# Kernel optimization log

Hardware: AMD Instinct MI355X
Metric: run time of the kernel (lower is better)

The kernel has to match this reference:

```python
import jax, jax.numpy as jnp
import numpy as np

NS = 6   # stuff classes
NT = 4   # thing classes
B, N, H, W, ROI = 2, 32, 768, 768, 28
C = NS + NT
NEG = -100.0


def setup_inputs():
    key = jax.random.key(0)
    k1, k2, k3, k4, k5, k6, k7 = jax.random.split(key, 7)
    sem_logits = jax.random.normal(k1, (B, C, H, W), dtype=jnp.float32)
    roi_msk_logits = jax.random.normal(k2, (B, N, NT, ROI, ROI), dtype=jnp.float32)
    y0 = jax.random.uniform(k3, (B, N), minval=0.0, maxval=H - 240.0)
    x0 = jax.random.uniform(k4, (B, N), minval=0.0, maxval=W - 240.0)
    hb = jax.random.uniform(k5, (B, N), minval=40.0, maxval=200.0)
    wb = jax.random.uniform(k6, (B, N), minval=40.0, maxval=200.0)
    bbx = jnp.stack([y0, x0, y0 + hb, x0 + wb], axis=-1).astype(jnp.float32)
    cls = jax.random.randint(k7, (B, N), 0, NT, dtype=jnp.int32)
    return {"sem_logits": sem_logits, "roi_msk_logits": roi_msk_logits, "bbx": bbx, "cls": cls}


def _fuse_logits(sem_logits, roi_msk_logits, bbx, cls):
    """Float part of Pofusion_ONNX.forward -> po_logits [B, NS+N, H, W]."""
    Bb, Cc, Hh, Ww = sem_logits.shape
    Nn = bbx.shape[1]
    R = roi_msk_logits.shape[-1]
    yy = jnp.arange(Hh)
    xx = jnp.arange(Ww)
    # per-box mask logits of its predicted class: [B,N,R,R]
    msk = jnp.take_along_axis(roi_msk_logits, cls[:, :, None, None, None], axis=2)[:, :, 0]
    stuff = sem_logits[:, :NS]  # [B,NS,H,W]
    y0 = jnp.floor(bbx[..., 0]).astype(jnp.int32)
    x0 = jnp.floor(bbx[..., 1]).astype(jnp.int32)
    y1 = jnp.floor(bbx[..., 2]).astype(jnp.int32)
    x1 = jnp.floor(bbx[..., 3]).astype(jnp.int32)
    # ---- po_process_semantic_logits: instance canvas (uses round()+1 on max corner) ----
    y1r = (jnp.round(bbx[..., 2]) + 1.0).astype(jnp.int32)
    x1r = (jnp.round(bbx[..., 3]) + 1.0).astype(jnp.int32)
    in_y_s = (yy[None, None, :] >= y0[..., None]) & (yy[None, None, :] < y1r[..., None])  # [B,N,H]
    in_x_s = (xx[None, None, :] >= x0[..., None]) & (xx[None, None, :] < x1r[..., None])  # [B,N,W]
    thing_logit = jnp.take_along_axis(sem_logits, (cls + NS)[:, :, None, None], axis=1)   # [B,N,H,W]
    inst = jnp.where(in_y_s[:, :, :, None] & in_x_s[:, :, None, :], thing_logit, NEG)
    # ---- po_process_mask_logits: bilinear resize (align_corners=False) + paste ----
    h = jnp.maximum(y1 - y0 + 1, 1).astype(jnp.float32)
    w = jnp.maximum(x1 - x0 + 1, 1).astype(jnp.float32)
    ys = jnp.maximum(y0, 0); ye = jnp.minimum(y1 + 1, Hh)
    xs = jnp.maximum(x0, 0); xe = jnp.minimum(x1 + 1, Ww)
    in_y_m = (yy[None, None, :] >= ys[..., None]) & (yy[None, None, :] < ye[..., None])
    in_x_m = (xx[None, None, :] >= xs[..., None]) & (xx[None, None, :] < xe[..., None])
    # source coords, PyTorch half-pixel convention with lower clamp at 0
    sy = (yy[None, None, :].astype(jnp.float32) - y0[..., None] + 0.5) * (R / h[..., None]) - 0.5
    sx = (xx[None, None, :].astype(jnp.float32) - x0[..., None] + 0.5) * (R / w[..., None]) - 0.5
    sy = jnp.clip(sy, 0.0, R - 1.0)
    sx = jnp.clip(sx, 0.0, R - 1.0)
    iy0 = jnp.floor(sy).astype(jnp.int32); iy1 = jnp.minimum(iy0 + 1, R - 1); wy = sy - iy0
    ix0 = jnp.floor(sx).astype(jnp.int32); ix1 = jnp.minimum(ix0 + 1, R - 1); wx = sx - ix0
    # separable bilinear: rows first (cheap [B,N,H,R] intermediate), then columns
    m0 = jnp.take_along_axis(msk, iy0[:, :, :, None], axis=2)
    m1 = jnp.take_along_axis(msk, iy1[:, :, :, None], axis=2)
    m_y = m0 * (1.0 - wy[..., None]) + m1 * wy[..., None]          # [B,N,H,R]
    c0 = jnp.take_along_axis(m_y, ix0[:, :, None, :], axis=3)
    c1 = jnp.take_along_axis(m_y, ix1[:, :, None, :], axis=3)
    resized = c0 * (1.0 - wx[:, :, None, :]) + c1 * wx[:, :, None, :]  # [B,N,H,W]
    mask_canvas = jnp.where(in_y_m[:, :, :, None] & in_x_m[:, :, None, :], resized, NEG)
    combined = (jax.nn.sigmoid(inst) + jax.nn.sigmoid(mask_canvas)) * (inst + mask_canvas)
    return jnp.concatenate([stuff, combined], axis=1)  # [B, NS+N, H, W]


def _post(po_logits, sem_logits, cls):
    """po_assign_class_label + po_generate_seamless_output (min_stuff_area=0)."""
    b3 = jnp.arange(B)[:, None, None]
    b2 = jnp.arange(B)[:, None]
    po_pred = jnp.argmax(po_logits, axis=1)   # argmax(softmax) == argmax(logits)
    sem_pred = jnp.argmax(sem_logits, axis=1)
    thing = po_pred >= NS
    k = jnp.clip(po_pred - NS, 0, N - 1)      # instance (box) id per pixel
    # per-instance histogram of sem_pred over its region (regions are disjoint)
    hist = jnp.zeros((B, N, C), jnp.int32).at[b3, k, sem_pred].add(thing.astype(jnp.int32))
    total = hist.sum(-1)
    present = total > 0
    sem_max = jnp.argmax(hist, axis=-1).astype(jnp.int32)  # first max == torch unique order
    max_cnt = hist.max(-1)
    tmp = cls + NS
    br1 = sem_max == tmp
    br2 = (~br1) & (2 * max_cnt >= total) & (sem_max < NS) & present  # max/total >= 0.5
    sem_label = jnp.where(br2, sem_max, tmp)
    kept = present & ~br2
    idx = jnp.cumsum(present.astype(jnp.int32), axis=1) - 1  # rank among present ids
    inst_label = jnp.where(kept, idx, -1)
    po_sem = jnp.where(thing, sem_label[b3, k], po_pred.astype(jnp.int32))
    po_inst = jnp.where(thing, inst_label[b3, k], -1)
    # ---- seamless output ----
    sp = jnp.zeros((B, NS), jnp.int32).at[b3, jnp.clip(po_sem, 0, NS - 1)].add((po_sem < NS).astype(jnp.int32))
    stuff_present = sp > 0
    stuff_rank = jnp.cumsum(stuff_present.astype(jnp.int32), axis=1) - 1
    n_stuff = stuff_present.sum(1).astype(jnp.int32)  # [B]
    v = jnp.where(kept, idx, N)
    present_v = (jnp.zeros((B, N + 1), jnp.int32).at[b2, v].add(1) > 0)[:, :N]
    rank_v = jnp.cumsum(present_v.astype(jnp.int32), axis=1) - 1
    seam_inst = 1 + n_stuff[:, None, None] + rank_v[b3, jnp.clip(po_inst, 0, N - 1)]
    seam_stuff = stuff_rank[b3, jnp.clip(po_sem, 0, NS - 1)] + 1
    seam = jnp.where(po_inst >= 0, seam_inst, jnp.where(po_sem < NS, seam_stuff, 0))
    po_pred_seamless = seam.reshape(B * H, W).astype(jnp.int32)  # torch cat over batch
    # padded class list [255, sorted stuff classes..., kept instance classes...]
    L = 1 + NS + N
    po_cls = jnp.full((B, L + 1), -1, jnp.int32).at[:, 0].set(255)
    stuff_pos = jnp.where(stuff_present, 1 + stuff_rank, L)  # L = dump slot
    po_cls = po_cls.at[b2, stuff_pos].set(jnp.broadcast_to(jnp.arange(NS, dtype=jnp.int32), (B, NS)))
    rank_k = jnp.cumsum(kept.astype(jnp.int32), axis=1) - 1
    inst_pos = jnp.where(kept, 1 + n_stuff[:, None] + rank_k, L)
    po_cls = po_cls.at[b2, inst_pos].set(tmp)
    po_cls = po_cls[:, :L]
    valid_len = (1 + n_stuff + kept.sum(1)).astype(jnp.int32)
    po_iscrowd = jnp.where(jnp.arange(L)[None, :] < valid_len[:, None], 0, -1).astype(jnp.int32)
    return po_pred_seamless, po_cls, po_iscrowd, valid_len


def reference(sem_logits, roi_msk_logits, bbx, cls):
    po_logits = _fuse_logits(sem_logits, roi_msk_logits, bbx, cls)
    return _post(po_logits, sem_logits, cls)
```

## Files before the change

kernel.cpp:

```cpp
#include <hip/hip_runtime.h>
#include <math.h>

#define NSs 6
#define NTs 4
#define Bb  2
#define Nn  32
#define Hh  768
#define Ww  768
#define Rr  28
#define Cch 10
#define NCH 38
#define HW  (Hh*Ww)
#define NEGD (-100.0)
#define NEGF (-100.0f)
#define NKEY (Nn*Cch + NSs)

struct InstP {
  int y0, x0, y1r, x1r;
  int ys, ye, xs, xe;
  float sc_y, sc_x;
  int tc;
  int mskoff;
};

__device__ __forceinline__ double sigd(double x) { return 1.0 / (1.0 + exp(-x)); }
__device__ __forceinline__ float  sigf(float x)  { return __fdividef(1.0f, 1.0f + __expf(-x)); }

__device__ __forceinline__ int fuse_px(
    int y, int x, const float (&ch)[Cch], unsigned rel,
    const InstP* __restrict__ spar, const float* __restrict__ roi,
    double EPS, int* smp_out)
{
  int smp = 0; float smv = ch[0];
#pragma unroll
  for (int c = 1; c < Cch; c++) if (ch[c] > smv) { smv = ch[c]; smp = c; }
  *smp_out = smp;

  double m = (double)ch[0]; int pidx = 0;
#pragma unroll
  for (int c = 1; c < NSs; c++) { double v = (double)ch[c]; if (v > m) { m = v; pidx = c; } }

  int next_ch = NSs;
  while (rel) {
    int n = __ffs(rel) - 1; rel &= rel - 1;
    int chn_ = NSs + n;
    if (chn_ > next_ch && EPS > m) { m = EPS; pidx = next_ch; }
    next_ch = chn_ + 1;
    const InstP p = spar[n];
    bool in_i = (y >= p.y0) && (y < p.y1r) && (x >= p.x0) && (x < p.x1r);
    bool in_m = (y >= p.ys) && (y < p.ye)  && (x >= p.xs) && (x < p.xe);
    bool in_any = in_i || in_m;
    if (__any(in_any)) {
      if (in_any) {
        int tcl = p.tc;
        float tl = (tcl == 6) ? ch[6] : (tcl == 7) ? ch[7] : (tcl == 8) ? ch[8] : ch[9];
        double iv = in_i ? (double)tl : NEGD;
        double mv = NEGD;
        if (in_m) {
          double syv = ((double)(y - p.y0) + 0.5) * (double)p.sc_y - 0.5;
          double sxv = ((double)(x - p.x0) + 0.5) * (double)p.sc_x - 0.5;
          syv = fmin(fmax(syv, 0.0), 27.0);
          sxv = fmin(fmax(sxv, 0.0), 27.0);
          int iy0 = (int)syv, ix0 = (int)sxv;
          int iy1 = min(iy0 + 1, 27), ix1 = min(ix0 + 1, 27);
          double wy = syv - (double)iy0, wx = sxv - (double)ix0;
          const float* mp = roi + p.mskoff;
          double m00 = (double)mp[iy0*Rr + ix0];
          double m01 = (double)mp[iy0*Rr + ix1];
          double m10 = (double)mp[iy1*Rr + ix0];
          double m11 = (double)mp[iy1*Rr + ix1];
          double c0 = m00*(1.0 - wy) + m10*wy;
          double c1 = m01*(1.0 - wy) + m11*wy;
          mv = c0*(1.0 - wx) + c1*wx;
        }
        double s2 = iv + mv;
        if (fmax(2.0*s2, 0.0) > m) {
          double val = (sigd(iv) + sigd(mv)) * s2;
          if (val > m) { m = val; pidx = chn_; }
        }
      } else {
        if (EPS > m) { m = EPS; pidx = chn_; }
      }
    } else {
      if (EPS > m) { m = EPS; pidx = chn_; }
    }
  }
  if (next_ch < NCH && EPS > m) { m = EPS; pidx = next_ch; }
  return pidx;
}

#define TOL_E 5e-4f
#define TOL_A 1e-3f
#define TOL_P 2e-3f

__device__ __forceinline__ int fuse_px_f32(
    int y, int x, const float (&ch)[Cch], unsigned rel,
    const InstP* __restrict__ spar, const float* __restrict__ roi,
    float EPSf, bool* certain)
{
  float m1 = ch[0]; int pidx = 0; bool wapprox = false;
  float m2x = -1e30f, m2a = -1e30f;

#define UPD_EXACT(v_, idx_) do { float _v = (v_); \
    if (_v > m1) { if (wapprox) m2a = fmaxf(m2a, m1); else m2x = fmaxf(m2x, m1); \
                   m1 = _v; pidx = (idx_); wapprox = false; } \
    else m2x = fmaxf(m2x, _v); } while (0)
#define UPD_APPROX(v_, idx_) do { float _v = (v_); \
    if (_v > m1) { if (wapprox) m2a = fmaxf(m2a, m1); else m2x = fmaxf(m2x, m1); \
                   m1 = _v; pidx = (idx_); wapprox = true; } \
    else m2a = fmaxf(m2a, _v); } while (0)

#pragma unroll
  for (int c = 1; c < NSs; c++) UPD_EXACT(ch[c], c);

  int next_ch = NSs;
  while (rel) {
    int n = __ffs(rel) - 1; rel &= rel - 1;
    int chn_ = NSs + n;
    if (chn_ > next_ch) UPD_EXACT(EPSf, next_ch);
    next_ch = chn_ + 1;
    const InstP p = spar[n];
    bool in_i = (y >= p.y0) && (y < p.y1r) && (x >= p.x0) && (x < p.x1r);
    bool in_m = (y >= p.ys) && (y < p.ye)  && (x >= p.xs) && (x < p.xe);
    bool in_any = in_i || in_m;
    if (__any(in_any)) {
      if (in_any) {
        int tcl = p.tc;
        float tl = (tcl == 6) ? ch[6] : (tcl == 7) ? ch[7] : (tcl == 8) ? ch[8] : ch[9];
        float iv = in_i ? tl : NEGF;
        float mv = NEGF;
        if (in_m) {
          float syv = ((float)(y - p.y0) + 0.5f) * p.sc_y - 0.5f;
          float sxv = ((float)(x - p.x0) + 0.5f) * p.sc_x - 0.5f;
          syv = fminf(fmaxf(syv, 0.0f), 27.0f);
          sxv = fminf(fmaxf(sxv, 0.0f), 27.0f);
          int iy0 = (int)syv, ix0 = (int)sxv;
          int iy1 = min(iy0 + 1, 27), ix1 = min(ix0 + 1, 27);
          float wy = syv - (float)iy0, wx = sxv - (float)ix0;
          const float* mp = roi + p.mskoff;
          float m00 = mp[iy0*Rr + ix0];
          float m01 = mp[iy0*Rr + ix1];
          float m10 = mp[iy1*Rr + ix0];
          float m11 = mp[iy1*Rr + ix1];
          float c0 = m00*(1.0f - wy) + m10*wy;
          float c1 = m01*(1.0f - wy) + m11*wy;
          mv = c0*(1.0f - wx) + c1*wx;
        }
        float s2 = iv + mv;
        if (fmaxf(2.0f*s2, 0.0f) > m1 - TOL_P) {
          float val = (sigf(iv) + sigf(mv)) * s2;
          UPD_APPROX(val, chn_);
        }
      } else {
        UPD_EXACT(EPSf, chn_);
      }
    } else {
      UPD_EXACT(EPSf, chn_);
    }
  }
  if (next_ch < NCH) UPD_EXACT(EPSf, next_ch);

  *certain = wapprox ? ((m1 - m2x > TOL_E) && (m1 - m2a > TOL_A))
                     : (m1 - m2a > TOL_E);
  return pidx;
#undef UPD_EXACT
#undef UPD_APPROX
}

__device__ __forceinline__ void setup_inst(
    int b, int n, const float* __restrict__ bbx, const int* __restrict__ cls,
    InstP* spar)
{
  const float* bbp = bbx + ((size_t)b*Nn + n)*4;
  float f0 = bbp[0], f1 = bbp[1], f2 = bbp[2], f3 = bbp[3];
  int y0 = (int)floorf(f0), x0 = (int)floorf(f1);
  int y1 = (int)floorf(f2), x1 = (int)floorf(f3);
  int y1r = (int)(rintf(f2) + 1.0f);
  int x1r = (int)(rintf(f3) + 1.0f);
  float hh = fmaxf((float)(y1 - y0 + 1), 1.0f);
  float wd = fmaxf((float)(x1 - x0 + 1), 1.0f);
  InstP p;
  p.y0 = y0; p.x0 = x0; p.y1r = y1r; p.x1r = x1r;
  p.ys = max(y0, 0); p.ye = min(y1 + 1, Hh);
  p.xs = max(x0, 0); p.xe = min(x1 + 1, Ww);
  p.sc_y = 28.0f / hh; p.sc_x = 28.0f / wd;
  int cl = cls[b*Nn + n];
  p.tc = NSs + cl;
  p.mskoff = (((b*Nn + n)*NTs) + cl)*Rr*Rr;
  spar[n] = p;
}

__global__ void k_zero(int* __restrict__ p, int n) {
  for (int i = threadIdx.x; i < n; i += 256) p[i] = 0;
}

__global__ __launch_bounds__(256) void k_fuse(
    const float* __restrict__ sem, const float* __restrict__ roi,
    const float* __restrict__ bbx, const int* __restrict__ cls,
    int* __restrict__ out_pred, int* __restrict__ g_hist, int* __restrict__ g_scount)
{
  __shared__ InstP spar[Nn];
  __shared__ int s_all[NKEY];
  __shared__ unsigned s_rel;
  __shared__ int s_xlo[Nn], s_xhi[Nn];

  const int bid  = blockIdx.x;
  const int y    = bid % Hh;
  const int b    = bid / Hh;
  const int tid  = threadIdx.x;
  const int lane = tid & 63;

  if (tid == 0) s_rel = 0u;
  for (int i = tid; i < NKEY; i += 256) s_all[i] = 0;
  if (tid < Nn) {
    setup_inst(b, tid, bbx, cls, spar);
    const InstP p = spar[tid];
    s_xlo[tid] = min(p.x0, p.xs);
    s_xhi[tid] = max(p.x1r, p.xe);
    bool rowi = (y >= p.y0) && (y < p.y1r);
    bool rowm = (y >= p.ys) && (y < p.ye);
    if (rowi || rowm) atomicOr(&s_rel, 1u << tid);
  }
  __syncthreads();

  const double EPS  = (sigd(NEGD) + sigd(NEGD)) * (NEGD + NEGD);
  const float  EPSf = (float)EPS;
  const float* base = sem + (size_t)b*Cch*HW + (size_t)y*Ww;

  const int  li   = lane & 31;
  const int  gxlo = s_xlo[li];
  const int  gxhi = s_xhi[li];
  const bool grow = (lane < 32) && ((s_rel >> li) & 1u);

  float cur[Cch], nxt[Cch];
#pragma unroll
  for (int c = 0; c < Cch; c++) cur[c] = base[(size_t)c*HW + tid];

  for (int ck = 0; ck < 3; ck++) {
    const int x = ck*256 + tid;
    if (ck < 2) {
#pragma unroll
      for (int c = 0; c < Cch; c++) nxt[c] = base[(size_t)c*HW + x + 256];
    }
    const int xa = x & ~63;
    unsigned relw = (unsigned)__ballot(grow && (gxlo < xa + 64) && (gxhi > xa));

    bool certain;
    int smp = 0;
    int pidx = fuse_px_f32(y, x, cur, relw, spar, roi, EPSf, &certain);
    if (!certain) {
      pidx = fuse_px(y, x, cur, relw, spar, roi, EPS, &smp);
    } else if (pidx >= NSs) {
      float smv = cur[0];
#pragma unroll
      for (int c = 1; c < Cch; c++) if (cur[c] > smv) { smv = cur[c]; smp = c; }
    }
    out_pred[(size_t)b*HW + (size_t)y*Ww + x] = pidx;
    atomicAdd(&s_all[(pidx >= NSs) ? ((pidx - NSs)*Cch + smp) : (Nn*Cch + pidx)], 1);

    if (ck < 2) {
#pragma unroll
      for (int c = 0; c < Cch; c++) cur[c] = nxt[c];
    }
  }

  __syncthreads();
  for (int i = tid; i < NKEY; i += 256) {
    int v = s_all[i];
    if (v) {
      if (i < Nn*Cch) atomicAdd(&g_hist[b*Nn*Cch + i], v);
      else            atomicAdd(&g_scount[b*NSs + (i - Nn*Cch)], v);
    }
  }
}

__global__ __launch_bounds__(256) void k_seam2(
    int* __restrict__ pred, const int* __restrict__ g_hist,
    const int* __restrict__ g_scount, const int* __restrict__ cls,
    int* __restrict__ out_tail)
{
  __shared__ int sh[Bb*Nn*Cch];
  __shared__ int spc_f[Bb][NSs];
  __shared__ int pcf[Bb][40];
  __shared__ int slut[Bb*NCH];
  const int t = threadIdx.x;
  for (int i = t; i < Bb*Nn*Cch; i += 256) sh[i] = g_hist[i];
  if (t < Bb*NSs) spc_f[t/NSs][t%NSs] = g_scount[t];
  __syncthreads();

  const int  b    = t >> 6;
  const int  lane = t & 63;
  const int  bs   = b & 1;
  const bool bv   = b < Bb;
  const bool act  = bv && (lane < Nn);

  int total = 0, mi = 0, mx = -1, tmp = 0;
  bool br2 = false, kept = false;
  if (act) {
    const int* hb = sh + b*Nn*Cch + lane*Cch;
#pragma unroll
    for (int c = 0; c < Cch; c++) { int v = hb[c]; total += v; if (v > mx) { mx = v; mi = c; } }
    tmp = cls[b*Nn + lane] + NSs;
    bool present = total > 0;
    bool b1 = (mi == tmp);
    br2  = (!b1) && (2*mx >= total) && (mi < NSs) && present;
    kept = present && !br2;
    if (br2) atomicAdd(&spc_f[b][mi], total);
  }
  __syncthreads();

  unsigned mask6 = (unsigned)(__ballot(bv && lane < NSs && spc_f[bs][lane] > 0) & 0x3Full);
  int nstuff = __popc(mask6);
  unsigned kmask = (unsigned)(__ballot(act && kept) & 0xFFFFFFFFull);
  int nk = __popc(kmask);
  int vlen = 1 + nstuff + nk;

  if (bv && lane < NSs)
    slut[b*NCH + lane] = __popc(mask6 & ((1u << lane) - 1)) + 1;
  if (act) {
    int rk     = __popc(kmask & ((1u << lane) - 1));
    int srk_mi = __popc(mask6 & ((1u << mi) - 1));
    slut[b*NCH + NSs + lane] = kept ? (1 + nstuff + rk) : (br2 ? srk_mi + 1 : 0);
  }
  if (bv && lane < 39) pcf[b][lane] = -1;
  __syncthreads();
  if (bv && lane == 0) pcf[b][0] = 255;
  if (bv && lane < NSs && ((mask6 >> lane) & 1))
    pcf[b][1 + __popc(mask6 & ((1u << lane) - 1))] = lane;
  if (act && kept)
    pcf[b][1 + nstuff + __popc(kmask & ((1u << lane) - 1))] = tmp;
  __syncthreads();

  if (blockIdx.x == 0) {
    int* pc = out_tail;
    int* ic = out_tail + Bb*39;
    int* vl = out_tail + 2*Bb*39;
    if (bv && lane < 39) {
      pc[b*39 + lane] = pcf[b][lane];
      ic[b*39 + lane] = (lane < vlen) ? 0 : -1;
    }
    if (bv && lane == 0) vl[b] = vlen;
  }

  size_t i = ((size_t)blockIdx.x*256 + t) * 4;
  int bb = (int)(i / HW);
  int4 v = *reinterpret_cast<int4*>(pred + i);
  int bo = bb*NCH;
  v.x = slut[bo + v.x];
  v.y = slut[bo + v.y];
  v.z = slut[bo + v.z];
  v.w = slut[bo + v.w];
  *reinterpret_cast<int4*>(pred + i) = v;
}

extern "C" void kernel_launch(void* const* d_in, const int* in_sizes, int n_in,
                              void* d_out, int out_size, void* d_ws, size_t ws_size,
                              hipStream_t stream)
{
  const float* sem = (const float*)d_in[0];
  const float* roi = (const float*)d_in[1];
  const float* bbx = (const float*)d_in[2];
  const int*   cls = (const int*)d_in[3];
  int* out = (int*)d_out;

  int* g_hist   = (int*)d_ws;
  int* g_scount = g_hist + Bb*Nn*Cch;

  k_zero<<<1, 256, 0, stream>>>(g_hist, Bb*Nn*Cch + Bb*NSs);
  k_fuse<<<dim3(Bb*Hh), 256, 0, stream>>>(sem, roi, bbx, cls, out, g_hist, g_scount);
  k_seam2<<<dim3((Bb*HW)/(256*4)), 256, 0, stream>>>(out, g_hist, g_scount, cls,
                                                     out + (size_t)Bb*HW);
}
```

Before: 111.6 us.

## Fuse zero, fuse and seam kernels into one cooperative kernel with grid syncs

```diff
diff --git a/kernel.cpp b/kernel.cpp
--- a/kernel.cpp
+++ b/kernel.cpp
@@ -1,5 +1,8 @@
 #include <hip/hip_runtime.h>
+#include <hip/hip_cooperative_groups.h>
 #include <math.h>
+
+namespace cg = cooperative_groups;
 
 #define NSs 6
 #define NTs 4
@@ -190,27 +193,16 @@
   spar[n] = p;
 }
 
-__global__ void k_zero(int* __restrict__ p, int n) {
-  for (int i = threadIdx.x; i < n; i += 256) p[i] = 0;
-}
-
-__global__ __launch_bounds__(256) void k_fuse(
+__device__ __forceinline__ void fuse_row_body(
+    int b, int y, int tid,
     const float* __restrict__ sem, const float* __restrict__ roi,
     const float* __restrict__ bbx, const int* __restrict__ cls,
-    int* __restrict__ out_pred, int* __restrict__ g_hist, int* __restrict__ g_scount)
-{
-  __shared__ InstP spar[Nn];
-  __shared__ int s_all[NKEY];
-  __shared__ unsigned s_rel;
-  __shared__ int s_xlo[Nn], s_xhi[Nn];
-
-  const int bid  = blockIdx.x;
-  const int y    = bid % Hh;
-  const int b    = bid / Hh;
-  const int tid  = threadIdx.x;
+    int* __restrict__ out_pred, int* __restrict__ g_hist, int* __restrict__ g_scount,
+    InstP* spar, int* s_all, unsigned* s_rel, int* s_xlo, int* s_xhi)
+{
   const int lane = tid & 63;
 
-  if (tid == 0) s_rel = 0u;
+  if (tid == 0) *s_rel = 0u;
   for (int i = tid; i < NKEY; i += 256) s_all[i] = 0;
   if (tid < Nn) {
     setup_inst(b, tid, bbx, cls, spar);
@@ -219,7 +211,7 @@
     s_xhi[tid] = max(p.x1r, p.xe);
     bool rowi = (y >= p.y0) && (y < p.y1r);
     bool rowm = (y >= p.ys) && (y < p.ye);
-    if (rowi || rowm) atomicOr(&s_rel, 1u << tid);
+    if (rowi || rowm) atomicOr(s_rel, 1u << tid);
   }
   __syncthreads();
 
@@ -230,7 +222,7 @@
   const int  li   = lane & 31;
   const int  gxlo = s_xlo[li];
   const int  gxhi = s_xhi[li];
-  const bool grow = (lane < 32) && ((s_rel >> li) & 1u);
+  const bool grow = (lane < 32) && ((*s_rel >> li) & 1u);
 
   float cur[Cch], nxt[Cch];
 #pragma unroll
@@ -272,6 +264,131 @@
       else            atomicAdd(&g_scount[b*NSs + (i - Nn*Cch)], v);
     }
   }
+}
+
+__global__ __launch_bounds__(256, 6) void k_all(
+    const float* __restrict__ sem, const float* __restrict__ roi,
+    const float* __restrict__ bbx, const int* __restrict__ cls,
+    int* __restrict__ out_pred, int* __restrict__ g_hist, int* __restrict__ g_scount,
+    int* __restrict__ out_tail)
+{
+  cg::grid_group grid = cg::this_grid();
+
+  __shared__ InstP spar[Nn];
+  __shared__ int s_all[NKEY];
+  __shared__ unsigned s_rel;
+  __shared__ int s_xlo[Nn], s_xhi[Nn];
+  __shared__ int sh[Bb*Nn*Cch];
+  __shared__ int spc_f[Bb][NSs];
+  __shared__ int pcf[Bb][40];
+  __shared__ int slut[Bb*NCH];
+
+  const int tid = threadIdx.x;
+  const int bid = blockIdx.x;
+  const int y   = bid % Hh;
+  const int b   = bid / Hh;
+
+  {
+    int g = bid*256 + tid;
+    if (g < Bb*Nn*Cch) g_hist[g] = 0;
+    else if (g < Bb*Nn*Cch + Bb*NSs) g_scount[g - Bb*Nn*Cch] = 0;
+  }
+  grid.sync();
+
+  fuse_row_body(b, y, tid, sem, roi, bbx, cls, out_pred, g_hist, g_scount,
+                spar, s_all, &s_rel, s_xlo, s_xhi);
+  grid.sync();
+
+  {
+    const int t = tid;
+    for (int i = t; i < Bb*Nn*Cch; i += 256) sh[i] = g_hist[i];
+    if (t < Bb*NSs) spc_f[t/NSs][t%NSs] = g_scount[t];
+    __syncthreads();
+
+    const int  bq  = t >> 6;
+    const int  ln  = t & 63;
+    const int  bsq = bq & 1;
+    const bool bv  = bq < Bb;
+    const bool act = bv && (ln < Nn);
+
+    int total = 0, mi = 0, mx = -1, tmp = 0;
+    bool br2 = false, kept = false;
+    if (act) {
+      const int* hb = sh + bq*Nn*Cch + ln*Cch;
+#pragma unroll
+      for (int c = 0; c < Cch; c++) { int v = hb[c]; total += v; if (v > mx) { mx = v; mi = c; } }
+      tmp = cls[bq*Nn + ln] + NSs;
+      bool present = total > 0;
+      bool b1 = (mi == tmp);
+      br2  = (!b1) && (2*mx >= total) && (mi < NSs) && present;
+      kept = present && !br2;
+      if (br2) atomicAdd(&spc_f[bq][mi], total);
+    }
+    __syncthreads();
+
+    unsigned mask6 = (unsigned)(__ballot(bv && ln < NSs && spc_f[bsq][ln] > 0) & 0x3Full);
+    int nstuff = __popc(mask6);
+    unsigned kmask = (unsigned)(__ballot(act && kept) & 0xFFFFFFFFull);
+    int nk = __popc(kmask);
+    int vlen = 1 + nstuff + nk;
+
+    if (bv && ln < NSs)
+      slut[bq*NCH + ln] = __popc(mask6 & ((1u << ln) - 1)) + 1;
+    if (act) {
+      int rk     = __popc(kmask & ((1u << ln) - 1));
+      int srk_mi = __popc(mask6 & ((1u << mi) - 1));
+      slut[bq*NCH + NSs + ln] = kept ? (1 + nstuff + rk) : (br2 ? srk_mi + 1 : 0);
+    }
+    if (bv && ln < 39) pcf[bq][ln] = -1;
+    __syncthreads();
+    if (bv && ln == 0) pcf[bq][0] = 255;
+    if (bv && ln < NSs && ((mask6 >> ln) & 1))
+      pcf[bq][1 + __popc(mask6 & ((1u << ln) - 1))] = ln;
+    if (act && kept)
+      pcf[bq][1 + nstuff + __popc(kmask & ((1u << ln) - 1))] = tmp;
+    __syncthreads();
+
+    if (bid == 0) {
+      int* pc = out_tail;
+      int* ic = out_tail + Bb*39;
+      int* vl = out_tail + 2*Bb*39;
+      if (bv && ln < 39) {
+        pc[bq*39 + ln] = pcf[bq][ln];
+        ic[bq*39 + ln] = (ln < vlen) ? 0 : -1;
+      }
+      if (bv && ln == 0) vl[bq] = vlen;
+    }
+
+    if (t < 192) {
+      int4* rowp = reinterpret_cast<int4*>(out_pred + (size_t)b*HW + (size_t)y*Ww);
+      int4 v = rowp[t];
+      int bo = b*NCH;
+      v.x = slut[bo + v.x];
+      v.y = slut[bo + v.y];
+      v.z = slut[bo + v.z];
+      v.w = slut[bo + v.w];
+      rowp[t] = v;
+    }
+  }
+}
+
+
+__global__ void k_zero(int* __restrict__ p, int n) {
+  for (int i = threadIdx.x; i < n; i += 256) p[i] = 0;
+}
+
+__global__ __launch_bounds__(256) void k_fuse(
+    const float* __restrict__ sem, const float* __restrict__ roi,
+    const float* __restrict__ bbx, const int* __restrict__ cls,
+    int* __restrict__ out_pred, int* __restrict__ g_hist, int* __restrict__ g_scount)
+{
+  __shared__ InstP spar[Nn];
+  __shared__ int s_all[NKEY];
+  __shared__ unsigned s_rel;
+  __shared__ int s_xlo[Nn], s_xhi[Nn];
+  const int bid = blockIdx.x;
+  fuse_row_body(bid / Hh, bid % Hh, threadIdx.x, sem, roi, bbx, cls,
+                out_pred, g_hist, g_scount, spar, s_all, &s_rel, s_xlo, s_xhi);
 }
 
 __global__ __launch_bounds__(256) void k_seam2(
@@ -365,9 +482,28 @@
 
   int* g_hist   = (int*)d_ws;
   int* g_scount = g_hist + Bb*Nn*Cch;
-
-  k_zero<<<1, 256, 0, stream>>>(g_hist, Bb*Nn*Cch + Bb*NSs);
-  k_fuse<<<dim3(Bb*Hh), 256, 0, stream>>>(sem, roi, bbx, cls, out, g_hist, g_scount);
-  k_seam2<<<dim3((Bb*HW)/(256*4)), 256, 0, stream>>>(out, g_hist, g_scount, cls,
-                                                     out + (size_t)Bb*HW);
-}
+  int* tailp    = out + (size_t)Bb*HW;
+
+  static int use_coop = -1;
+  if (use_coop < 0) {
+    int maxB = 0;
+    hipError_t e1 = hipOccupancyMaxActiveBlocksPerMultiprocessor(
+        &maxB, reinterpret_cast<const void*>(k_all), 256, 0);
+    int dev = 0; (void)hipGetDevice(&dev);
+    hipDeviceProp_t prop;
+    hipError_t e2 = hipGetDeviceProperties(&prop, dev);
+    use_coop = (e1 == hipSuccess && e2 == hipSuccess &&
+                (long)maxB * prop.multiProcessorCount >= (long)Bb*Hh) ? 1 : 0;
+  }
+
+  if (use_coop) {
+    void* args[] = { (void*)&sem, (void*)&roi, (void*)&bbx, (void*)&cls,
+                     (void*)&out, (void*)&g_hist, (void*)&g_scount, (void*)&tailp };
+    hipLaunchCooperativeKernel(reinterpret_cast<const void*>(k_all),
+                               dim3(Bb*Hh), dim3(256), args, 0, stream);
+  } else {
+    k_zero<<<1, 256, 0, stream>>>(g_hist, Bb*Nn*Cch + Bb*NSs);
+    k_fuse<<<dim3(Bb*Hh), 256, 0, stream>>>(sem, roi, bbx, cls, out, g_hist, g_scount);
+    k_seam2<<<dim3((Bb*HW)/(256*4)), 256, 0, stream>>>(out, g_hist, g_scount, cls, tailp);
+  }
+}
```

After: 110.0 us. No clear change (-1.4%).
